# Performance work log

Hardware: AMD Instinct MI355X
Metric: run time of the kernel (lower is better)

## Reference

```python
import jax, jax.numpy as jnp
import numpy as np

EPS = 1e-05
N = 8192


def setup_inputs() -> dict:
    key = jax.random.key(0)
    k1, k2 = jax.random.split(key)
    params = jax.random.normal(k1, (3,), dtype=jnp.float32) * 0.1
    # sparse-ish symmetric 0/1 adjacency, float32 like the torch buffer
    a = (jax.random.uniform(k2, (N, N)) < 0.005).astype(jnp.float32)
    graph = jnp.maximum(a, a.T)
    return {"params": params, "graph": graph}


def reference(params, graph):
    alpha, beta, sigma = params[0], params[1], params[2]
    n = graph.shape[0]
    # p == 0 => sum_degrees(v) is just the degree (row sum) of v
    deg = jnp.sum(graph, axis=1)                       # [n]
    s = alpha * deg[:, None] + beta * deg[None, :] + sigma   # [n, n]
    p = 1.0 / (1.0 + jnp.exp(s))                        # logistic prob
    ll = jnp.where(graph == 1.0,
                   jnp.log(p + EPS),
                   jnp.log(1.0 - p + EPS))
    # loop runs over i <= j: upper triangle including diagonal
    upper = jnp.triu(jnp.ones((n, n), dtype=bool))
    likelihood = jnp.sum(jnp.where(upper, ll, 0.0))
    return -likelihood
```

## Files before the change

kernel.cpp:

```cpp
#include <hip/hip_runtime.h>

#define N 8192
#define EPS 1e-5f
#define LOG2E 1.4426950408889634f
#define LN2d  0.6931471805599453

#define TR 64
#define TC 256
#define NBJ 32
#define NBI 128
#define RPW 16
#define CAPW 512
#define SEG_W 4096
#define NTILES 2112
#define NSEG (NTILES * 4)
#define NDENSE 4096
#define NFB 1024

static const size_t OFF_ACC = 0;
static const size_t OFF_DEG = 4096;
static const size_t OFF_CNT = OFF_DEG + (size_t)N * 4;
static const size_t OFF_EDG = OFF_CNT + (size_t)NSEG * 4;
static const size_t WS_NEED = OFF_EDG + (size_t)NSEG * SEG_W * 4;

__device__ __forceinline__ unsigned mbcnt64(unsigned long long m) {
    return __builtin_amdgcn_mbcnt_hi((unsigned)(m >> 32),
           __builtin_amdgcn_mbcnt_lo((unsigned)m, 0u));
}

__global__ __launch_bounds__(256) void k_pass1(const float* __restrict__ g,
        float* __restrict__ deg, unsigned* __restrict__ cnt,
        unsigned* __restrict__ edges, const int segmode) {
    const int bj = (int)blockIdx.x & (NBJ - 1);
    const int bi = (int)blockIdx.x >> 5;
    if (bi > 4 * bj + 3) return;
    const int r0 = bi * TR, c0 = bj * TC;
    const int wave = threadIdx.x >> 6, lane = threadIdx.x & 63;
    const int aid = 2 * bj * (bj + 1) + bi;

    __shared__ float    scol[TC];
    __shared__ unsigned buf[4][CAPW];
    scol[threadIdx.x] = 0.f;
    __syncthreads();

    const int c = c0 + lane * 4;
    const int rbase = r0 + wave * RPW;
    const float* __restrict__ gp = g + (size_t)rbase * N + c;
    unsigned* __restrict__ myseg = edges + ((size_t)aid * 4 + wave) * SEG_W;
    unsigned wc = 0, wflushed = 0;
    float ca0 = 0.f, ca1 = 0.f, ca2 = 0.f, ca3 = 0.f;

#define EMIT(BB, PRED, OFFv) \
    if (BB) { if (segmode && (PRED)) buf[wave][wc + mbcnt64(BB)] = etag | (OFFv); \
        const unsigned p_ = __popcll(BB); wc += p_; rsum += p_; }

#define FLUSHCHK \
    if (segmode && wc > (unsigned)(CAPW - 256)) { \
        for (unsigned t_ = lane; t_ < wc; t_ += 64) myseg[wflushed + t_] = buf[wave][t_]; \
        wflushed += wc; wc = 0; }

    if (r0 + TR <= c0) {
        #pragma unroll 4
        for (int k = 0; k < RPW; ++k) {
            const float4 v = *reinterpret_cast<const float4*>(gp + (size_t)k * N);
            FLUSHCHK
            ca0 += v.x; ca1 += v.y; ca2 += v.z; ca3 += v.w;
            const unsigned long long b0 = __ballot(v.x != 0.f);
            const unsigned long long b1 = __ballot(v.y != 0.f);
            const unsigned long long b2 = __ballot(v.z != 0.f);
            const unsigned long long b3 = __ballot(v.w != 0.f);
            if (b0 | b1 | b2 | b3) {
                const int gr = rbase + k;
                const unsigned etag = ((unsigned)gr << 16) | (unsigned)c;
                unsigned rsum = 0;
                EMIT(b0, v.x != 0.f, 0u)
                EMIT(b1, v.y != 0.f, 1u)
                EMIT(b2, v.z != 0.f, 2u)
                EMIT(b3, v.w != 0.f, 3u)
                if (lane == 0) atomicAdd(&deg[gr], (float)rsum);
            }
        }
    } else {
        for (int k = 0; k < RPW; ++k) {
            const int gr = rbase + k;
            const float4 v = *reinterpret_cast<const float4*>(gp + (size_t)k * N);
            FLUSHCHK
            const bool a0 = (v.x != 0.f) && (c + 0 >= gr);
            const bool a1 = (v.y != 0.f) && (c + 1 >= gr);
            const bool a2 = (v.z != 0.f) && (c + 2 >= gr);
            const bool a3 = (v.w != 0.f) && (c + 3 >= gr);
            ca0 += (c + 0 > gr) ? v.x : 0.f;
            ca1 += (c + 1 > gr) ? v.y : 0.f;
            ca2 += (c + 2 > gr) ? v.z : 0.f;
            ca3 += (c + 3 > gr) ? v.w : 0.f;
            const unsigned long long b0 = __ballot(a0);
            const unsigned long long b1 = __ballot(a1);
            const unsigned long long b2 = __ballot(a2);
            const unsigned long long b3 = __ballot(a3);
            if (b0 | b1 | b2 | b3) {
                const unsigned etag = ((unsigned)gr << 16) | (unsigned)c;
                unsigned rsum = 0;
                EMIT(b0, a0, 0u)
                EMIT(b1, a1, 1u)
                EMIT(b2, a2, 2u)
                EMIT(b3, a3, 3u)
                if (lane == 0) atomicAdd(&deg[gr], (float)rsum);
            }
        }
    }
#undef EMIT
#undef FLUSHCHK

    if (segmode) {
        for (unsigned t = lane; t < wc; t += 64) myseg[wflushed + t] = buf[wave][t];
        if (lane == 0) cnt[aid * 4 + wave] = wflushed + wc;
    }
    if (ca0 != 0.f) atomicAdd(&scol[lane * 4 + 0], ca0);
    if (ca1 != 0.f) atomicAdd(&scol[lane * 4 + 1], ca1);
    if (ca2 != 0.f) atomicAdd(&scol[lane * 4 + 2], ca2);
    if (ca3 != 0.f) atomicAdd(&scol[lane * 4 + 3], ca3);
    __syncthreads();
    const float sv = scol[threadIdx.x];
    if (sv != 0.f) atomicAdd(&deg[c0 + threadIdx.x], sv);
}

__global__ __launch_bounds__(256) void k_ll(const float* __restrict__ g,
        const float* __restrict__ deg, const float* __restrict__ params,
        const unsigned* __restrict__ cnt, const unsigned* __restrict__ edges,
        double* __restrict__ accv, const int segmode) {
    const int b = blockIdx.x;
    const float alpha = params[0], beta = params[1], sigma = params[2];
    double dlocal = 0.0;

    if (b < NDENSE) {
        if (!segmode) return;
        const int r1 = b, r2 = N - 1 - b;
        const float b2 = beta * LOG2E;
        const float base1 = fmaf(alpha, deg[r1], sigma) * LOG2E;
        const float base2 = fmaf(alpha, deg[r2], sigma) * LOG2E;
        float l0 = 0.f, l1 = 0.f, l2 = 0.f, l3 = 0.f;
        float l4 = 0.f, l5 = 0.f, l6 = 0.f, l7 = 0.f;

#define DELEM(J, ACC, BASE) { \
        const float s2_ = fmaf(b2, deg[J], BASE); \
        const float e_  = __builtin_amdgcn_exp2f(s2_); \
        const float p_  = __builtin_amdgcn_rcpf(1.f + e_); \
        ACC += __builtin_amdgcn_logf(1.00001f - p_); }

        int j = r1 + (int)threadIdx.x;
        for (; j + 1792 < N; j += 2048) {
            DELEM(j,        l0, base1)
            DELEM(j + 256,  l1, base1)
            DELEM(j + 512,  l2, base1)
            DELEM(j + 768,  l3, base1)
            DELEM(j + 1024, l4, base1)
            DELEM(j + 1280, l5, base1)
            DELEM(j + 1536, l6, base1)
            DELEM(j + 1792, l7, base1)
        }
        for (; j < N; j += 256) DELEM(j, l0, base1)

        j = r2 + (int)threadIdx.x;
        for (; j + 1792 < N; j += 2048) {
            DELEM(j,        l0, base2)
            DELEM(j + 256,  l1, base2)
            DELEM(j + 512,  l2, base2)
            DELEM(j + 768,  l3, base2)
            DELEM(j + 1024, l4, base2)
            DELEM(j + 1280, l5, base2)
            DELEM(j + 1536, l6, base2)
            DELEM(j + 1792, l7, base2)
        }
        for (; j < N; j += 256) DELEM(j, l1, base2)
#undef DELEM
        dlocal = (double)(((l0 + l1) + (l2 + l3)) + ((l4 + l5) + (l6 + l7))) * LN2d;
    } else if (b < NDENSE + NTILES) {
        if (!segmode) return;
        const int aid = b - NDENSE;
        float local = 0.f;
        for (int w = 0; w < 4; ++w) {
            const unsigned n = cnt[aid * 4 + w];
            const unsigned* __restrict__ seg = edges + ((size_t)aid * 4 + w) * SEG_W;
            for (unsigned t = threadIdx.x; t < n; t += 256) {
                const unsigned e = seg[t];
                const float di = deg[e >> 16];
                const float dj = deg[e & 0xffffu];
                const float s = fmaf(alpha, di, fmaf(beta, dj, sigma));
                const float p = __fdividef(1.f, 1.f + __expf(s));
                local += __logf(p + EPS) - __logf(1.f - p + EPS);
            }
        }
        dlocal = (double)local;
    } else {
        if (segmode) return;
        const int rb = b - NDENSE - NTILES;
        for (int q = 0; q < 8; ++q) {
            const int i = rb * 8 + q;
            const float base = fmaf(alpha, deg[i], sigma);
            float rl = 0.f;
            for (int j = i + (int)threadIdx.x; j < N; j += 256) {
                const float s = fmaf(beta, deg[j], base);
                const float p = __fdividef(1.f, 1.f + __expf(s));
                const float gv = g[(size_t)i * N + j];
                rl += (gv != 0.f) ? __logf(p + EPS) : __logf(1.f - p + EPS);
            }
            dlocal += (double)rl;
        }
    }

    #pragma unroll
    for (int off = 32; off; off >>= 1) dlocal += __shfl_xor(dlocal, off);
    __shared__ double wsum[4];
    const int wv = threadIdx.x >> 6, ln = threadIdx.x & 63;
    if (ln == 0) wsum[wv] = dlocal;
    __syncthreads();
    if (threadIdx.x == 0) {
        const double t = (wsum[0] + wsum[1]) + (wsum[2] + wsum[3]);
        if (t != 0.0) atomicAdd(&accv[(b & 63) * 8], t);
    }
}

__global__ void k_final(const double* __restrict__ accv, float* __restrict__ out) {
    double v = accv[threadIdx.x * 8];
    #pragma unroll
    for (int off = 32; off; off >>= 1) v += __shfl_xor(v, off);
    if (threadIdx.x == 0) out[0] = (float)(-v);
}

extern "C" void kernel_launch(void* const* d_in, const int* in_sizes, int n_in,
                              void* d_out, int out_size, void* d_ws, size_t ws_size,
                              hipStream_t stream) {
    const float* params = (const float*)d_in[0];
    const float* graph  = (const float*)d_in[1];
    float* out = (float*)d_out;

    char* ws = (char*)d_ws;
    double*   accv  = (double*)(ws + OFF_ACC);
    float*    deg   = (float*)(ws + OFF_DEG);
    unsigned* cnt   = (unsigned*)(ws + OFF_CNT);
    unsigned* edges = (unsigned*)(ws + OFF_EDG);
    const int segmode = (ws_size >= WS_NEED) ? 1 : 0;

    hipMemsetAsync(ws, 0, OFF_DEG + (size_t)N * 4, stream);
    k_pass1<<<NBI * NBJ, 256, 0, stream>>>(graph, deg, cnt, edges, segmode);
    const int llgrid = segmode ? (NDENSE + NTILES) : (NDENSE + NTILES + NFB);
    k_ll<<<llgrid, 256, 0, stream>>>(graph, deg, params, cnt, edges, accv, segmode);
    k_final<<<1, 64, 0, stream>>>(accv, out);
}
```

Before: 60.28 us.

## Replace dense transcendental evaluation with per-row degree lookup tables in LDS

In the dense upper-triangle blocks, the code first finds the min and max degree over the row range, then precomputes log(1-p) for every integer degree value into a shared-memory table for both paired rows. The main loops then replace exp/rcp/log per element with a table lookup indexed by the degree, which cuts transcendental work since degrees span a small range. It adds a min/max reduction pass over deg, an extra block barrier and LDS usage, and falls back to direct evaluation if the range exceeds the table size. Degrees are assumed to be integers, which holds for a 0/1 adjacency.

```diff
diff --git a/kernel.cpp b/kernel.cpp
--- a/kernel.cpp
+++ b/kernel.cpp
@@ -16,6 +16,7 @@
 #define NSEG (NTILES * 4)
 #define NDENSE 4096
 #define NFB 1024
+#define TBLMAX 1024
 
 static const size_t OFF_ACC = 0;
 static const size_t OFF_DEG = 4096;
@@ -128,6 +129,11 @@
         const float* __restrict__ deg, const float* __restrict__ params,
         const unsigned* __restrict__ cnt, const unsigned* __restrict__ edges,
         double* __restrict__ accv, const int segmode) {
+    __shared__ float  tbl[2][TBLMAX];
+    __shared__ double wsum[4];
+    __shared__ float  rmn[4], rmx[4];
+    const int tid = threadIdx.x;
+    const int wv = tid >> 6, ln = tid & 63;
     const int b = blockIdx.x;
     const float alpha = params[0], beta = params[1], sigma = params[2];
     double dlocal = 0.0;
@@ -138,42 +144,72 @@
         const float b2 = beta * LOG2E;
         const float base1 = fmaf(alpha, deg[r1], sigma) * LOG2E;
         const float base2 = fmaf(alpha, deg[r2], sigma) * LOG2E;
+
+        float mn = 3.0e38f, mx = -3.0e38f;
+        for (int j = r1 + tid; j < N; j += 256) {
+            const float d = deg[j];
+            mn = fminf(mn, d); mx = fmaxf(mx, d);
+        }
+        #pragma unroll
+        for (int off = 32; off; off >>= 1) {
+            mn = fminf(mn, __shfl_xor(mn, off));
+            mx = fmaxf(mx, __shfl_xor(mx, off));
+        }
+        if (ln == 0) { rmn[wv] = mn; rmx[wv] = mx; }
+        __syncthreads();
+        mn = fminf(fminf(rmn[0], rmn[1]), fminf(rmn[2], rmn[3]));
+        mx = fmaxf(fmaxf(rmx[0], rmx[1]), fmaxf(rmx[2], rmx[3]));
+        const int dmin = (int)mn;
+        const int R = (int)mx - dmin + 1;
+
+#define DEVAL(DV, BASE) \
+        __builtin_amdgcn_logf(1.00001f - __builtin_amdgcn_rcpf(1.f + \
+            __builtin_amdgcn_exp2f(fmaf(b2, (DV), (BASE)))))
+
         float l0 = 0.f, l1 = 0.f, l2 = 0.f, l3 = 0.f;
-        float l4 = 0.f, l5 = 0.f, l6 = 0.f, l7 = 0.f;
-
-#define DELEM(J, ACC, BASE) { \
-        const float s2_ = fmaf(b2, deg[J], BASE); \
-        const float e_  = __builtin_amdgcn_exp2f(s2_); \
-        const float p_  = __builtin_amdgcn_rcpf(1.f + e_); \
-        ACC += __builtin_amdgcn_logf(1.00001f - p_); }
-
-        int j = r1 + (int)threadIdx.x;
-        for (; j + 1792 < N; j += 2048) {
-            DELEM(j,        l0, base1)
-            DELEM(j + 256,  l1, base1)
-            DELEM(j + 512,  l2, base1)
-            DELEM(j + 768,  l3, base1)
-            DELEM(j + 1024, l4, base1)
-            DELEM(j + 1280, l5, base1)
-            DELEM(j + 1536, l6, base1)
-            DELEM(j + 1792, l7, base1)
-        }
-        for (; j < N; j += 256) DELEM(j, l0, base1)
-
-        j = r2 + (int)threadIdx.x;
-        for (; j + 1792 < N; j += 2048) {
-            DELEM(j,        l0, base2)
-            DELEM(j + 256,  l1, base2)
-            DELEM(j + 512,  l2, base2)
-            DELEM(j + 768,  l3, base2)
-            DELEM(j + 1024, l4, base2)
-            DELEM(j + 1280, l5, base2)
-            DELEM(j + 1536, l6, base2)
-            DELEM(j + 1792, l7, base2)
-        }
-        for (; j < N; j += 256) DELEM(j, l1, base2)
-#undef DELEM
-        dlocal = (double)(((l0 + l1) + (l2 + l3)) + ((l4 + l5) + (l6 + l7))) * LN2d;
+        if (R <= TBLMAX) {
+            for (int i = tid; i < R; i += 256) {
+                const float dv = (float)(dmin + i);
+                tbl[0][i] = DEVAL(dv, base1);
+                tbl[1][i] = DEVAL(dv, base2);
+            }
+            __syncthreads();
+            int j = r1 + tid;
+            for (; j + 768 < N; j += 1024) {
+                l0 += tbl[0][(int)deg[j]       - dmin];
+                l1 += tbl[0][(int)deg[j + 256] - dmin];
+                l2 += tbl[0][(int)deg[j + 512] - dmin];
+                l3 += tbl[0][(int)deg[j + 768] - dmin];
+            }
+            for (; j < N; j += 256) l0 += tbl[0][(int)deg[j] - dmin];
+            j = r2 + tid;
+            for (; j + 768 < N; j += 1024) {
+                l0 += tbl[1][(int)deg[j]       - dmin];
+                l1 += tbl[1][(int)deg[j + 256] - dmin];
+                l2 += tbl[1][(int)deg[j + 512] - dmin];
+                l3 += tbl[1][(int)deg[j + 768] - dmin];
+            }
+            for (; j < N; j += 256) l0 += tbl[1][(int)deg[j] - dmin];
+        } else {
+            int j = r1 + tid;
+            for (; j + 768 < N; j += 1024) {
+                l0 += DEVAL(deg[j], base1);
+                l1 += DEVAL(deg[j + 256], base1);
+                l2 += DEVAL(deg[j + 512], base1);
+                l3 += DEVAL(deg[j + 768], base1);
+            }
+            for (; j < N; j += 256) l0 += DEVAL(deg[j], base1);
+            j = r2 + tid;
+            for (; j + 768 < N; j += 1024) {
+                l0 += DEVAL(deg[j], base2);
+                l1 += DEVAL(deg[j + 256], base2);
+                l2 += DEVAL(deg[j + 512], base2);
+                l3 += DEVAL(deg[j + 768], base2);
+            }
+            for (; j < N; j += 256) l0 += DEVAL(deg[j], base2);
+        }
+#undef DEVAL
+        dlocal = (double)((l0 + l1) + (l2 + l3)) * LN2d;
     } else if (b < NDENSE + NTILES) {
         if (!segmode) return;
         const int aid = b - NDENSE;
@@ -181,7 +217,7 @@
         for (int w = 0; w < 4; ++w) {
             const unsigned n = cnt[aid * 4 + w];
             const unsigned* __restrict__ seg = edges + ((size_t)aid * 4 + w) * SEG_W;
-            for (unsigned t = threadIdx.x; t < n; t += 256) {
+            for (unsigned t = tid; t < n; t += 256) {
                 const unsigned e = seg[t];
                 const float di = deg[e >> 16];
                 const float dj = deg[e & 0xffffu];
@@ -198,7 +234,7 @@
             const int i = rb * 8 + q;
             const float base = fmaf(alpha, deg[i], sigma);
             float rl = 0.f;
-            for (int j = i + (int)threadIdx.x; j < N; j += 256) {
+            for (int j = i + tid; j < N; j += 256) {
                 const float s = fmaf(beta, deg[j], base);
                 const float p = __fdividef(1.f, 1.f + __expf(s));
                 const float gv = g[(size_t)i * N + j];
@@ -210,11 +246,9 @@
 
     #pragma unroll
     for (int off = 32; off; off >>= 1) dlocal += __shfl_xor(dlocal, off);
-    __shared__ double wsum[4];
-    const int wv = threadIdx.x >> 6, ln = threadIdx.x & 63;
     if (ln == 0) wsum[wv] = dlocal;
     __syncthreads();
-    if (threadIdx.x == 0) {
+    if (tid == 0) {
         const double t = (wsum[0] + wsum[1]) + (wsum[2] + wsum[3]);
         if (t != 0.0) atomicAdd(&accv[(b & 63) * 8], t);
     }
```

After: 66.59 us. 1.1x slower.
